# Optimization experiments

Hardware: AMD Instinct MI355X
Metric: run time of the kernel (lower is better)

Reference implementation:

```python
import jax, jax.numpy as jnp
import numpy as np

B, N, C, H, P = 16, 4096, 256, 4, 64  # batch, tokens, hidden, heads, proj_size
HD = C // H  # head dim = 64
EPS = 1e-12  # torch F.normalize eps


def _l2norm(t):
    # normalize along last axis, torch-style: t / max(||t||, eps)
    n = jnp.sqrt(jnp.sum(t * t, axis=-1, keepdims=True))
    return t / jnp.maximum(n, EPS)


def setup_inputs() -> dict:
    key = jax.random.key(0)
    ks = jax.random.split(key, 12)
    s = 0.02
    return {
        "x": jax.random.normal(ks[0], (B, N, C), jnp.float32),
        "ref": jax.random.normal(ks[1], (B, N, C), jnp.float32),
        "Wq": jax.random.normal(ks[2], (C, C), jnp.float32) * s,
        "bq": jnp.zeros((C,), jnp.float32),
        "Wkvv": jax.random.normal(ks[3], (3 * C, C), jnp.float32) * s,
        "bkvv": jnp.zeros((3 * C,), jnp.float32),
        "WE": jax.random.normal(ks[4], (P, N), jnp.float32) * s,  # E and F share weights
        "bE": jnp.zeros((P,), jnp.float32),
        "Wo1": jax.random.normal(ks[5], (C // 2, C), jnp.float32) * s,
        "bo1": jnp.zeros((C // 2,), jnp.float32),
        "Wo2": jax.random.normal(ks[6], (C // 2, C), jnp.float32) * s,
        "bo2": jnp.zeros((C // 2,), jnp.float32),
        "temp": jnp.ones((H, 1, 1), jnp.float32),
        "temp2": jnp.ones((H, 1, 1), jnp.float32),
    }


def reference(x, ref, Wq, bq, Wkvv, bkvv, WE, bE, Wo1, bo1, Wo2, bo2, temp, temp2):
    b, n, c = x.shape
    hd = c // H
    # q projection -> [B,H,hd,N] (already transposed so channel dim first)
    q = (x @ Wq.T + bq).reshape(b, n, H, hd).transpose(0, 2, 3, 1)
    kvv = (ref @ Wkvv.T + bkvv).reshape(b, n, 3, H, hd).transpose(2, 0, 3, 4, 1)
    k, v_ca, v_sa = kvv[0], kvv[1], kvv[2]
    # L2 normalize over token axis (last)
    qn = _l2norm(q)
    kn = _l2norm(k)
    # ---- channel attention (XCA-style): [B,H,hd,hd]
    attn_ca = jax.nn.softmax(jnp.einsum('bhcn,bhdn->bhcd', qn, kn) * temp, axis=-1)
    x_ca = jnp.einsum('bhcd,bhdn->bhcn', attn_ca, v_ca)  # [B,H,hd,N]
    x_ca = x_ca.transpose(0, 3, 1, 2).reshape(b, n, c)   # [B,N,C]
    # ---- spatial attention with Linformer-style projection (E == F shared)
    k_proj = kn @ WE.T + bE      # [B,H,hd,P]
    v_proj = v_sa @ WE.T + bE    # [B,H,hd,P]
    attn_sa = jax.nn.softmax(jnp.einsum('bhcn,bhcp->bhnp', qn, k_proj) * temp2, axis=-1)
    x_sa = jnp.einsum('bhnp,bhcp->bhnc', attn_sa, v_proj)  # [B,H,N,hd]
    # faithful to original permute(0,3,1,2).reshape(B,N,C)
    x_sa = x_sa.transpose(0, 3, 1, 2).reshape(b, n, c)
    # output projections + concat (SA first, then CA)
    out_ca = x_ca @ Wo1.T + bo1
    out_sa = x_sa @ Wo2.T + bo2
    return jnp.concatenate((out_sa, out_ca), axis=-1)
```

## Files before the change

### kernel.cpp

```cpp
#include <hip/hip_runtime.h>
#include <hip/hip_bf16.h>

#define DI __device__ __forceinline__

constexpr int B_ = 16, N_ = 4096, C_ = 256, H_ = 4;
constexpr size_t QSZ = (size_t)4096 * 4096;
constexpr int LDW = 72;
constexpr int LDC = 136;

typedef __attribute__((ext_vector_type(8))) short bh8;
typedef __attribute__((ext_vector_type(4))) float fx4;
typedef __attribute__((address_space(1))) unsigned int gu32;
typedef __attribute__((address_space(3))) unsigned int lu32;

DI float bfu2f(unsigned short u) { return __uint_as_float(((unsigned)u) << 16); }
DI void bfu2x2(unsigned u, float& lo, float& hi) {
  lo = __uint_as_float(u << 16);
  hi = __uint_as_float(u & 0xffff0000u);
}
DI unsigned short f2bfu(float f) {
  unsigned u = __float_as_uint(f);
  unsigned r = 0x7fffu + ((u >> 16) & 1u);
  return (unsigned short)((u + r) >> 16);
}
DI void gl_lds16(const unsigned short* g, unsigned short* l) {
  __builtin_amdgcn_global_load_lds((gu32*)g, (lu32*)l, 16, 0, 0);
}
DI int co_off(int row, int col) {
  const int o = col >> 3;
  const int so = (o & 8) | ((o & 7) ^ ((row >> 3) & 7));
  return row * LDC + so * 8 + (col & 7);
}

__global__ __launch_bounds__(256) void cast_xref(
    const float* __restrict__ x, const float* __restrict__ ref,
    unsigned short* __restrict__ xb, unsigned short* __restrict__ refb)
{
  const int bid = blockIdx.x;
  const float* src = (bid < 8192) ? x : ref;
  unsigned short* dst = (bid < 8192) ? xb : refb;
  const size_t base = ((size_t)(bid & 8191) * 256 + threadIdx.x) * 8;
  const float4 a = *reinterpret_cast<const float4*>(&src[base]);
  const float4 b = *reinterpret_cast<const float4*>(&src[base + 4]);
  union { uint4 v; unsigned short u[8]; } pk;
  pk.u[0] = f2bfu(a.x); pk.u[1] = f2bfu(a.y); pk.u[2] = f2bfu(a.z); pk.u[3] = f2bfu(a.w);
  pk.u[4] = f2bfu(b.x); pk.u[5] = f2bfu(b.y); pk.u[6] = f2bfu(b.z); pk.u[7] = f2bfu(b.w);
  *reinterpret_cast<uint4*>(&dst[base]) = pk.v;
}

__global__ __launch_bounds__(256) void cast_w(
    const float* __restrict__ Wq, const float* __restrict__ Wkvv,
    const float* __restrict__ Wo2, const float* __restrict__ Wo1,
    const float* __restrict__ WE, unsigned short* __restrict__ Wb,
    unsigned short* __restrict__ wEb)
{
  const int b = blockIdx.x;
  const float* src; unsigned short* dst; int lb;
  if (b < 32)       { src = Wq;   dst = Wb;          lb = b; }
  else if (b < 128) { src = Wkvv; dst = Wb + 65536;  lb = b - 32; }
  else if (b < 144) { src = Wo2;  dst = Wb + 262144; lb = b - 128; }
  else if (b < 160) { src = Wo1;  dst = Wb + 294912; lb = b - 144; }
  else              { src = WE;   dst = wEb;         lb = b - 160; }
  const size_t base = ((size_t)lb * 256 + threadIdx.x) * 8;
  const float4 a = *reinterpret_cast<const float4*>(&src[base]);
  const float4 bb = *reinterpret_cast<const float4*>(&src[base + 4]);
  union { uint4 v; unsigned short u[8]; } pk;
  pk.u[0] = f2bfu(a.x);  pk.u[1] = f2bfu(a.y);  pk.u[2] = f2bfu(a.z);  pk.u[3] = f2bfu(a.w);
  pk.u[4] = f2bfu(bb.x); pk.u[5] = f2bfu(bb.y); pk.u[6] = f2bfu(bb.z); pk.u[7] = f2bfu(bb.w);
  *reinterpret_cast<uint4*>(&dst[base]) = pk.v;
}

__global__ __launch_bounds__(256) void proj_fused(
    const unsigned short* __restrict__ xb, const unsigned short* __restrict__ refb,
    const unsigned short* __restrict__ Wball,
    const float* __restrict__ bq, const float* __restrict__ bkvv,
    unsigned short* __restrict__ qT, unsigned short* __restrict__ kvv2T,
    unsigned short* __restrict__ qtok, unsigned short* __restrict__ vtok)
{
  __shared__ unsigned short smem[17408];
  __shared__ float biasS[128];
  const int tid = threadIdx.x;
  const int lane = tid & 63, wid = tid >> 6;
  const int l15 = lane & 15, l4 = lane >> 4;
  const int wr = wid >> 1, wc = wid & 1;
  const int yt = blockIdx.y;
  const bool isq = (yt < 2);
  const unsigned short* Ab = isq ? xb : refb;
  const unsigned short* Wsrc = isq ? Wball : (Wball + 65536);
  const float* bias = isq ? bq : bkvv;
  unsigned short* outT = isq ? qT : kvv2T;
  const int j0 = (isq ? yt : (yt - 2)) * 128;
  const int pl = j0 >> 8;
  const bool writeT = isq || (pl != 1);
  const int plT = (!isq && pl == 2) ? 1 : 0;
  unsigned short* tok = isq ? qtok : ((pl == 1) ? vtok : nullptr);
  const int n0 = blockIdx.x * 128;
  const int b = blockIdx.z;
  const size_t tok0 = (size_t)b * 4096 + n0;
  const int lrow = lane >> 3, lcb = lane & 7;
  if (tid < 128) biasS[tid] = bias[j0 + tid];

  fx4 acc[4][4];
#pragma unroll
  for (int m = 0; m < 4; ++m)
#pragma unroll
    for (int n = 0; n < 4; ++n) acc[m][n] = (fx4){0.f, 0.f, 0.f, 0.f};

  auto STAGE = [&](int k0) {
    unsigned short* Wd = smem;
    unsigned short* Xd = smem + 8192;
#pragma unroll
    for (int i = 0; i < 4; ++i) {
      const int ci = i * 4 + wid;
      const int row = ci * 8 + lrow;
      const int scb = lcb ^ (row & 7);
      gl_lds16(&Wsrc[(size_t)(j0 + row) * 256 + k0 + scb * 8], &Wd[ci * 512]);
      gl_lds16(&Ab[(tok0 + row) * 256 + k0 + scb * 8], &Xd[ci * 512]);
    }
  };
  auto COMPUTE = [&]() {
    const unsigned short* Ws = smem;
    const unsigned short* Xs = smem + 8192;
#pragma unroll
    for (int kk = 0; kk < 2; ++kk) {
      const int cbi = kk * 4 + l4;
      bh8 af[4], bfr[4];
#pragma unroll
      for (int m = 0; m < 4; ++m) {
        const int r = wr * 64 + m * 16 + l15;
        af[m] = *reinterpret_cast<const bh8*>(&Ws[r * 64 + ((cbi ^ (r & 7)) << 3)]);
      }
#pragma unroll
      for (int n = 0; n < 4; ++n) {
        const int r = wc * 64 + n * 16 + l15;
        bfr[n] = *reinterpret_cast<const bh8*>(&Xs[r * 64 + ((cbi ^ (r & 7)) << 3)]);
      }
#pragma unroll
      for (int m = 0; m < 4; ++m)
#pragma unroll
        for (int n = 0; n < 4; ++n)
          acc[m][n] = __builtin_amdgcn_mfma_f32_16x16x32_bf16(af[m], bfr[n], acc[m][n], 0, 0, 0);
    }
  };

  for (int t = 0; t < 4; ++t) {
    STAGE(t * 64);
    __syncthreads();
    COMPUTE();
    __syncthreads();
  }

  unsigned short* Co = smem;
#pragma unroll
  for (int m = 0; m < 4; ++m) {
    const int jl = wr * 64 + m * 16 + (l4 << 2);
#pragma unroll
    for (int n = 0; n < 4; ++n) {
      const int col = wc * 64 + n * 16 + l15;
#pragma unroll
      for (int r = 0; r < 4; ++r) {
        const int row = jl + r;
        Co[co_off(row, col)] = f2bfu(acc[m][n][r] + biasS[row]);
      }
    }
  }
  __syncthreads();
  if (writeT) {
#pragma unroll
    for (int c = 0; c < 8; ++c) {
      const int r = c * 16 + (tid >> 4);
      const int colseg = (tid & 15) * 8;
      const uint4 v = *reinterpret_cast<const uint4*>(&Co[co_off(r, colseg)]);
      const int jj = j0 + r;
      const int rowT = (plT * B_ + b) * 256 + (jj & 255);
      *reinterpret_cast<uint4*>(&outT[(size_t)rowT * N_ + n0 + colseg]) = v;
    }
  }
  if (tok) {
    const int j = tid & 7;
#pragma unroll
    for (int i = 0; i < 8; ++i) {
      const int half = i >> 2;
      const int cb = half * 64 + j * 8;
      const int nloc = (i & 3) * 32 + (tid >> 3);
      union { uint4 v; unsigned short u[8]; } pk;
#pragma unroll
      for (int t = 0; t < 8; ++t)
        pk.u[t] = Co[co_off(cb + t, nloc)];
      const int jj = j0 + cb;
      const int hh = (jj >> 6) & 3, cc = jj & 63;
      *reinterpret_cast<uint4*>(
          &tok[(((size_t)b * 4 + hh) * 4096 + n0 + nloc) * 64 + cc]) = pk.v;
    }
  }
}

__global__ __launch_bounds__(256) void gemm_outm2(
    const unsigned short* __restrict__ Asa, const unsigned short* __restrict__ Aca,
    const unsigned short* __restrict__ Wob,
    const float* __restrict__ bo2, const float* __restrict__ bo1,
    float* __restrict__ out)
{
  __shared__ unsigned short smem[16384];
  __shared__ float biasS[128];
  const unsigned short* A = (blockIdx.z == 0) ? Asa : Aca;
  const unsigned short* Wsrc = Wob + (size_t)blockIdx.z * 32768;
  const float* bias = (blockIdx.z == 0) ? bo2 : bo1;
  const int joff = blockIdx.z * 128;
  const int tid = threadIdx.x;
  const int lane = tid & 63, wid = tid >> 6;
  const int l15 = lane & 15, l4 = lane >> 4;
  const int wr = wid >> 1, wc = wid & 1;
  const size_t m0 = (size_t)blockIdx.x * 128;
  const int lrow = lane >> 3, lcb = lane & 7;
  if (tid < 128) biasS[tid] = bias[tid];

  fx4 acc[4][4];
#pragma unroll
  for (int m = 0; m < 4; ++m)
#pragma unroll
    for (int n = 0; n < 4; ++n) acc[m][n] = (fx4){0.f, 0.f, 0.f, 0.f};

  auto STAGE = [&](int k0) {
    unsigned short* Wd = smem;
    unsigned short* Xd = smem + 8192;
#pragma unroll
    for (int i = 0; i < 4; ++i) {
      const int ci = i * 4 + wid;
      const int row = ci * 8 + lrow;
      const int scb = lcb ^ (row & 7);
      gl_lds16(&Wsrc[(size_t)row * 256 + k0 + scb * 8], &Wd[ci * 512]);
      gl_lds16(&A[(m0 + row) * 256 + k0 + scb * 8], &Xd[ci * 512]);
    }
  };
  auto COMPUTE = [&]() {
    const unsigned short* Ws = smem;
    const unsigned short* Xs = smem + 8192;
#pragma unroll
    for (int kk = 0; kk < 2; ++kk) {
      const int cbi = kk * 4 + l4;
      bh8 af[4], bfr[4];
#pragma unroll
      for (int m = 0; m < 4; ++m) {
        const int r = wr * 64 + m * 16 + l15;
        af[m] = *reinterpret_cast<const bh8*>(&Xs[r * 64 + ((cbi ^ (r & 7)) << 3)]);
      }
#pragma unroll
      for (int n = 0; n < 4; ++n) {
        const int r = wc * 64 + n * 16 + l15;
        bfr[n] = *reinterpret_cast<const bh8*>(&Ws[r * 64 + ((cbi ^ (r & 7)) << 3)]);
      }
#pragma unroll
      for (int m = 0; m < 4; ++m)
#pragma unroll
        for (int n = 0; n < 4; ++n)
          acc[m][n] = __builtin_amdgcn_mfma_f32_16x16x32_bf16(af[m], bfr[n], acc[m][n], 0, 0, 0);
    }
  };

  for (int t = 0; t < 4; ++t) {
    STAGE(t * 64);
    __syncthreads();
    COMPUTE();
    __syncthreads();
  }

#pragma unroll
  for (int mi = 0; mi < 4; ++mi) {
    const int mrow = wr * 64 + mi * 16 + (l4 << 2);
#pragma unroll
    for (int ni = 0; ni < 4; ++ni) {
      const int j = wc * 64 + ni * 16 + l15;
      const float bv = biasS[j];
#pragma unroll
      for (int r = 0; r < 4; ++r)
        out[(m0 + mrow + r) * 256 + joff + j] = acc[mi][ni][r] + bv;
    }
  }
}

__global__ __launch_bounds__(256) void stats_mfma(
    const unsigned short* __restrict__ qT, const unsigned short* __restrict__ kT,
    const unsigned short* __restrict__ vT, const unsigned short* __restrict__ wEb,
    float* __restrict__ part, float* __restrict__ partN)
{
  __shared__ unsigned short smem[4 * 64 * LDW];
  unsigned short* sq = smem;
  unsigned short* sk = smem + 64 * LDW;
  unsigned short* sv = smem + 2 * 64 * LDW;
  unsigned short* sw = smem + 3 * 64 * LDW;
  const int tid = threadIdx.x;
  const int lane = tid & 63, wid = tid >> 6;
  const int bh = blockIdx.x, chunk = blockIdx.y;
  const size_t rowbase = (size_t)bh * 64 * N_;

  fx4 acc[4][4];
#pragma unroll
  for (int m = 0; m < 4; ++m)
#pragma unroll
    for (int n = 0; n < 4; ++n) acc[m][n] = (fx4){0.f, 0.f, 0.f, 0.f};
  float q2 = 0.f, k2 = 0.f;

  const unsigned short* Aop = (wid == 1) ? sw : (wid == 2) ? sv : sq;
  const unsigned short* Bop = (wid == 1) ? sk : (wid == 2) ? sw : sk;

  for (int tile = 0; tile < 8; ++tile) {
    const int n0 = chunk * 512 + tile * 64;
#pragma unroll
    for (int c = 0; c < 2; ++c) {
      const int idx = c * 256 + tid;
      const int r = idx >> 3;
      const int off = (idx & 7) * 8;
      *reinterpret_cast<uint4*>(&sq[r * LDW + off]) =
          *reinterpret_cast<const uint4*>(&qT[rowbase + (size_t)r * N_ + n0 + off]);
      *reinterpret_cast<uint4*>(&sk[r * LDW + off]) =
          *reinterpret_cast<const uint4*>(&kT[rowbase + (size_t)r * N_ + n0 + off]);
      *reinterpret_cast<uint4*>(&sv[r * LDW + off]) =
          *reinterpret_cast<const uint4*>(&vT[rowbase + (size_t)r * N_ + n0 + off]);
      *reinterpret_cast<uint4*>(&sw[r * LDW + off]) =
          *reinterpret_cast<const uint4*>(&wEb[(size_t)r * N_ + n0 + off]);
    }
    __syncthreads();
    if (wid < 3) {
#pragma unroll
      for (int kk = 0; kk < 2; ++kk) {
        const int kb = kk * 32 + (lane >> 4) * 8;
        bh8 af[4], bfr[4];
#pragma unroll
        for (int m = 0; m < 4; ++m)
          af[m] = *reinterpret_cast<const bh8*>(&Aop[(m * 16 + (lane & 15)) * LDW + kb]);
#pragma unroll
        for (int n = 0; n < 4; ++n)
          bfr[n] = *reinterpret_cast<const bh8*>(&Bop[(n * 16 + (lane & 15)) * LDW + kb]);
#pragma unroll
        for (int m = 0; m < 4; ++m)
#pragma unroll
          for (int n = 0; n < 4; ++n)
            acc[m][n] = __builtin_amdgcn_mfma_f32_16x16x32_bf16(af[m], bfr[n], acc[m][n], 0, 0, 0);
      }
    } else {
      const unsigned short* qrow = &sq[lane * LDW];
      const unsigned short* krow = &sk[lane * LDW];
#pragma unroll
      for (int t = 0; t < 8; ++t) {
        const uint4 uq = *reinterpret_cast<const uint4*>(&qrow[t * 8]);
        const uint4 uk = *reinterpret_cast<const uint4*>(&krow[t * 8]);
        float a, b;
        bfu2x2(uq.x, a, b); q2 += a * a + b * b;
        bfu2x2(uq.y, a, b); q2 += a * a + b * b;
        bfu2x2(uq.z, a, b); q2 += a * a + b * b;
        bfu2x2(uq.w, a, b); q2 += a * a + b * b;
        bfu2x2(uk.x, a, b); k2 += a * a + b * b;
        bfu2x2(uk.y, a, b); k2 += a * a + b * b;
        bfu2x2(uk.z, a, b); k2 += a * a + b * b;
        bfu2x2(uk.w, a, b); k2 += a * a + b * b;
      }
    }
    __syncthreads();
  }

  if (wid < 3) {
    float* base = &part[(((size_t)chunk * 64 + bh) * 3 + wid) * 4096];
#pragma unroll
    for (int m = 0; m < 4; ++m) {
      const int row0 = m * 16 + ((lane >> 4) << 2);
#pragma unroll
      for (int n = 0; n < 4; ++n) {
        const int col = n * 16 + (lane & 15);
#pragma unroll
        for (int r = 0; r < 4; ++r)
          base[(row0 + r) * 64 + col] = acc[m][n][r];
      }
    }
  } else {
    float* nb = &partN[((size_t)chunk * 64 + bh) * 128];
    nb[lane] = q2;
    nb[64 + lane] = k2;
  }
}

__global__ __launch_bounds__(256) void postproc_kernel(
    const float* __restrict__ part, const float* __restrict__ partN,
    const float* __restrict__ bE,
    const float* __restrict__ temp, const float* __restrict__ temp2,
    unsigned short* __restrict__ attn_b,
    unsigned short* __restrict__ kp2t, unsigned short* __restrict__ vpb)
{
  __shared__ float sums[12288];
  __shared__ float rqS[64], rkS[64];
  const int bh = blockIdx.x;
  const int tid = threadIdx.x;
  for (int idx = tid; idx < 12288; idx += 256) {
    float s = 0.f;
    for (int ch = 0; ch < 8; ++ch)
      s += part[((size_t)ch * 64 + bh) * 12288 + idx];
    sums[idx] = s;
  }
  if (tid < 128) {
    float s = 0.f;
    for (int ch = 0; ch < 8; ++ch)
      s += partN[((size_t)ch * 64 + bh) * 128 + tid];
    const float r = 1.f / fmaxf(sqrtf(s), 1e-12f);
    if (tid < 64) rqS[tid] = r; else rkS[tid - 64] = r;
  }
  __syncthreads();
  const float t2 = temp2[bh & 3];
  for (int idx = tid; idx < 4096; idx += 256) {
    const int p = idx >> 6, c = idx & 63;
    kp2t[(size_t)bh * 4096 + idx] =
        f2bfu((sums[4096 + idx] * rkS[c] + bE[p]) * rqS[c] * t2);
    vpb[(size_t)bh * 4096 + idx] = f2bfu(sums[8192 + idx] + bE[idx & 63]);
  }
  const float tv = temp[bh & 3];
  const int lane = tid & 63, wv = tid >> 6;
  for (int ri = 0; ri < 16; ++ri) {
    const int c = wv * 16 + ri;
    const float val = sums[c * 64 + lane] * rqS[c] * rkS[lane] * tv;
    float m = val;
#pragma unroll
    for (int off = 32; off > 0; off >>= 1) m = fmaxf(m, __shfl_xor(m, off));
    const float e = __expf(val - m);
    float ssum = e;
#pragma unroll
    for (int off = 32; off > 0; off >>= 1) ssum += __shfl_xor(ssum, off);
    attn_b[(size_t)bh * 4096 + c * 64 + lane] = f2bfu(e / ssum);
  }
}

__global__ __launch_bounds__(256) void sa_mfma(
    const unsigned short* __restrict__ qtok, const unsigned short* __restrict__ kp2t,
    const unsigned short* __restrict__ vpb, unsigned short* __restrict__ x_sa)
{
  __shared__ unsigned short skp[64 * LDW];
  __shared__ unsigned short svp[64 * LDW];
  __shared__ unsigned short pt[4][64 * LDW];
  const int tid = threadIdx.x;
  const int lane = tid & 63, wid = tid >> 6;
  const int l15 = lane & 15, l4 = lane >> 4;
  const int bh = blockIdx.x, b = bh >> 2, h = bh & 3;
  const int n0 = blockIdx.y * 256 + wid * 64;
  unsigned short* myp = &pt[wid][0];

#pragma unroll
  for (int i = 0; i < 2; ++i) {
    const int idx = i * 256 + tid;
    const int r = idx >> 3, off = (idx & 7) * 8;
    *reinterpret_cast<uint4*>(&skp[r * LDW + off]) =
        *reinterpret_cast<const uint4*>(&kp2t[(size_t)bh * 4096 + r * 64 + off]);
    *reinterpret_cast<uint4*>(&svp[r * LDW + off]) =
        *reinterpret_cast<const uint4*>(&vpb[(size_t)bh * 4096 + r * 64 + off]);
  }
  __syncthreads();

  fx4 acc[4][4];
#pragma unroll
  for (int m = 0; m < 4; ++m)
#pragma unroll
    for (int j = 0; j < 4; ++j) acc[m][j] = (fx4){0.f, 0.f, 0.f, 0.f};
  const size_t qbase = ((size_t)bh * 4096 + n0) * 64;
#pragma unroll
  for (int kk = 0; kk < 2; ++kk) {
    const int kb = kk * 32 + l4 * 8;
    bh8 af[4], bf[4];
#pragma unroll
    for (int m = 0; m < 4; ++m)
      af[m] = *reinterpret_cast<const bh8*>(&qtok[qbase + (size_t)(m * 16 + l15) * 64 + kb]);
#pragma unroll
    for (int j = 0; j < 4; ++j)
      bf[j] = *reinterpret_cast<const bh8*>(&skp[(j * 16 + l15) * LDW + kb]);
#pragma unroll
    for (int m = 0; m < 4; ++m)
#pragma unroll
      for (int j = 0; j < 4; ++j)
        acc[m][j] = __builtin_amdgcn_mfma_f32_16x16x32_bf16(af[m], bf[j], acc[m][j], 0, 0, 0);
  }

  fx4 inv[4];
#pragma unroll
  for (int m = 0; m < 4; ++m) {
    fx4 vm = acc[m][0];
#pragma unroll
    for (int j = 1; j < 4; ++j)
#pragma unroll
      for (int r = 0; r < 4; ++r) vm[r] = fmaxf(vm[r], acc[m][j][r]);
#pragma unroll
    for (int msk = 1; msk < 16; msk <<= 1)
#pragma unroll
      for (int r = 0; r < 4; ++r) vm[r] = fmaxf(vm[r], __shfl_xor(vm[r], msk));
    fx4 s = (fx4){0.f, 0.f, 0.f, 0.f};
#pragma unroll
    for (int j = 0; j < 4; ++j)
#pragma unroll
      for (int r = 0; r < 4; ++r) {
        acc[m][j][r] = __expf(acc[m][j][r] - vm[r]);
        s[r] += acc[m][j][r];
      }
#pragma unroll
    for (int msk = 1; msk < 16; msk <<= 1)
#pragma unroll
      for (int r = 0; r < 4; ++r) s[r] += __shfl_xor(s[r], msk);
#pragma unroll
    for (int r = 0; r < 4; ++r) inv[m][r] = 1.f / s[r];
#pragma unroll
    for (int j = 0; j < 4; ++j)
#pragma unroll
      for (int r = 0; r < 4; ++r)
        myp[(m * 16 + l4 * 4 + r) * LDW + j * 16 + l15] = f2bfu(acc[m][j][r]);
  }

  fx4 acc2[4][4];
#pragma unroll
  for (int m = 0; m < 4; ++m)
#pragma unroll
    for (int j = 0; j < 4; ++j) acc2[m][j] = (fx4){0.f, 0.f, 0.f, 0.f};
#pragma unroll
  for (int kk = 0; kk < 2; ++kk) {
    const int kb = kk * 32 + l4 * 8;
    bh8 af[4], bf[4];
#pragma unroll
    for (int m = 0; m < 4; ++m)
      af[m] = *reinterpret_cast<const bh8*>(&myp[(m * 16 + l15) * LDW + kb]);
#pragma unroll
    for (int j = 0; j < 4; ++j)
      bf[j] = *reinterpret_cast<const bh8*>(&svp[(j * 16 + l15) * LDW + kb]);
#pragma unroll
    for (int m = 0; m < 4; ++m)
#pragma unroll
      for (int j = 0; j < 4; ++j)
        acc2[m][j] = __builtin_amdgcn_mfma_f32_16x16x32_bf16(af[m], bf[j], acc2[m][j], 0, 0, 0);
  }

#pragma unroll
  for (int m = 0; m < 4; ++m)
#pragma unroll
    for (int j = 0; j < 4; ++j)
#pragma unroll
      for (int r = 0; r < 4; ++r)
        myp[(m * 16 + l4 * 4 + r) * 65 + j * 16 + l15] = f2bfu(acc2[m][j][r] * inv[m][r]);
#pragma unroll
  for (int dstep = 0; dstep < 8; ++dstep) {
    const int d = dstep * 8 + (lane >> 3);
    const int nseg = (lane & 7) * 8;
    union { uint4 v; unsigned short u[8]; } pk;
#pragma unroll
    for (int t = 0; t < 8; ++t) pk.u[t] = myp[(nseg + t) * 65 + d];
    *reinterpret_cast<uint4*>(
        &x_sa[((size_t)(b * 64 + d) * 4 + h) * (size_t)N_ + n0 + nseg]) = pk.v;
  }
}

__global__ __launch_bounds__(256) void xca_mfma(
    const unsigned short* __restrict__ attn_b, const unsigned short* __restrict__ vtok,
    unsigned short* __restrict__ x_ca)
{
  __shared__ unsigned short co[4][64 * LDW];
  const int tid = threadIdx.x;
  const int lane = tid & 63, wid = tid >> 6;
  const int l15 = lane & 15, l4 = lane >> 4;
  const int bh = blockIdx.x, b = bh >> 2, h = bh & 3;
  const int n0 = blockIdx.y * 256 + wid * 64;
  unsigned short* myco = &co[wid][0];

  fx4 acc[4][4];
#pragma unroll
  for (int m = 0; m < 4; ++m)
#pragma unroll
    for (int j = 0; j < 4; ++j) acc[m][j] = (fx4){0.f, 0.f, 0.f, 0.f};
  const size_t abase = (size_t)bh * 4096;
  const size_t vbase = ((size_t)bh * 4096 + n0) * 64;
#pragma unroll
  for (int kk = 0; kk < 2; ++kk) {
    const int kb = kk * 32 + l4 * 8;
    bh8 af[4], bf[4];
#pragma unroll
    for (int m = 0; m < 4; ++m)
      af[m] = *reinterpret_cast<const bh8*>(&attn_b[abase + (size_t)(m * 16 + l15) * 64 + kb]);
#pragma unroll
    for (int j = 0; j < 4; ++j)
      bf[j] = *reinterpret_cast<const bh8*>(&vtok[vbase + (size_t)(j * 16 + l15) * 64 + kb]);
#pragma unroll
    for (int m = 0; m < 4; ++m)
#pragma unroll
      for (int j = 0; j < 4; ++j)
        acc[m][j] = __builtin_amdgcn_mfma_f32_16x16x32_bf16(af[m], bf[j], acc[m][j], 0, 0, 0);
  }

#pragma unroll
  for (int m = 0; m < 4; ++m)
#pragma unroll
    for (int j = 0; j < 4; ++j)
#pragma unroll
      for (int r = 0; r < 4; ++r)
        myco[(j * 16 + l15) * LDW + m * 16 + l4 * 4 + r] = f2bfu(acc[m][j][r]);
#pragma unroll
  for (int p = 0; p < 8; ++p) {
    const int nloc = p * 8 + (lane >> 3);
    const int cseg = (lane & 7) * 8;
    const uint4 v = *reinterpret_cast<const uint4*>(&myco[nloc * LDW + cseg]);
    *reinterpret_cast<uint4*>(
        &x_ca[((size_t)b * N_ + n0 + nloc) * 256 + h * 64 + cseg]) = v;
  }
}

extern "C" void kernel_launch(void* const* d_in, const int* in_sizes, int n_in,
                              void* d_out, int out_size, void* d_ws, size_t ws_size,
                              hipStream_t stream)
{
  const float* x     = (const float*)d_in[0];
  const float* ref   = (const float*)d_in[1];
  const float* Wq    = (const float*)d_in[2];
  const float* bq    = (const float*)d_in[3];
  const float* Wkvv  = (const float*)d_in[4];
  const float* bkvv  = (const float*)d_in[5];
  const float* WE    = (const float*)d_in[6];
  const float* bE    = (const float*)d_in[7];
  const float* Wo1   = (const float*)d_in[8];
  const float* bo1   = (const float*)d_in[9];
  const float* Wo2   = (const float*)d_in[10];
  const float* bo2   = (const float*)d_in[11];
  const float* temp  = (const float*)d_in[12];
  const float* temp2 = (const float*)d_in[13];
  float* out = (float*)d_out;

  char* ws = (char*)d_ws;
  unsigned short* qT      = (unsigned short*)(ws);
  unsigned short* kvv2T   = (unsigned short*)(ws + 33554432);
  unsigned short* qtok    = (unsigned short*)(ws + 100663296);
  unsigned short* refb    = (unsigned short*)(ws + 134217728);
  unsigned short* x_sa    = (unsigned short*)(ws + 134217728);
  unsigned short* vca_tok = (unsigned short*)(ws + 167772160);
  unsigned short* xb      = (unsigned short*)(ws + 201326592);
  float*          part    = (float*)(ws + 201326592);
  unsigned short* x_ca    = (unsigned short*)(ws + 201326592);
  float*          partN   = (float*)(ws + 226492416);
  unsigned short* Wb      = (unsigned short*)(ws + 234881024);
  unsigned short* wEb     = (unsigned short*)(ws + 235536384);
  unsigned short* attn_b  = (unsigned short*)(ws + 236093440);
  unsigned short* kp2t    = (unsigned short*)(ws + 236617728);
  unsigned short* vpb     = (unsigned short*)(ws + 237142016);

  const dim3 blk(256);
  cast_xref<<<dim3(16384), blk, 0, stream>>>(x, ref, xb, refb);
  cast_w<<<dim3(288), blk, 0, stream>>>(Wq, Wkvv, Wo2, Wo1, WE, Wb, wEb);
  proj_fused<<<dim3(32, 8, 16), blk, 0, stream>>>(xb, refb, Wb, bq, bkvv,
                                                  qT, kvv2T, qtok, vca_tok);
  stats_mfma<<<dim3(64, 8), blk, 0, stream>>>(qT, kvv2T, kvv2T + QSZ, wEb, part, partN);
  postproc_kernel<<<dim3(64), blk, 0, stream>>>(part, partN, bE, temp, temp2,
                                                attn_b, kp2t, vpb);
  sa_mfma<<<dim3(64, 16), blk, 0, stream>>>(qtok, kp2t, vpb, x_sa);
  xca_mfma<<<dim3(64, 16), blk, 0, stream>>>(attn_b, vca_tok, x_ca);
  gemm_outm2<<<dim3(512, 1, 2), blk, 0, stream>>>(x_sa, x_ca, Wb + 262144, bo2, bo1, out);
}
```

Measured before the change: 205.2 us.

## Merge cast kernels and remap projection grid for XCD-aware L2 reuse

The two fp32-to-bf16 cast kernels become one launch covering activations and weights, which removes one kernel launch. The projection GEMM switches from a 3D grid to a 1D grid. Its block index is decoded so that the eight output-column tiles for the same token tile land on the same XCD, which should let them share that XCD's L2 for the input tile. The index remap is arithmetic only, but a wrong decode would silently produce a partial result.

```diff
diff --git a/kernel.cpp b/kernel.cpp
--- a/kernel.cpp
+++ b/kernel.cpp
@@ -32,35 +32,26 @@
   return row * LDC + so * 8 + (col & 7);
 }
 
-__global__ __launch_bounds__(256) void cast_xref(
+__global__ __launch_bounds__(256) void cast_all(
     const float* __restrict__ x, const float* __restrict__ ref,
-    unsigned short* __restrict__ xb, unsigned short* __restrict__ refb)
-{
-  const int bid = blockIdx.x;
-  const float* src = (bid < 8192) ? x : ref;
-  unsigned short* dst = (bid < 8192) ? xb : refb;
-  const size_t base = ((size_t)(bid & 8191) * 256 + threadIdx.x) * 8;
-  const float4 a = *reinterpret_cast<const float4*>(&src[base]);
-  const float4 b = *reinterpret_cast<const float4*>(&src[base + 4]);
-  union { uint4 v; unsigned short u[8]; } pk;
-  pk.u[0] = f2bfu(a.x); pk.u[1] = f2bfu(a.y); pk.u[2] = f2bfu(a.z); pk.u[3] = f2bfu(a.w);
-  pk.u[4] = f2bfu(b.x); pk.u[5] = f2bfu(b.y); pk.u[6] = f2bfu(b.z); pk.u[7] = f2bfu(b.w);
-  *reinterpret_cast<uint4*>(&dst[base]) = pk.v;
-}
-
-__global__ __launch_bounds__(256) void cast_w(
     const float* __restrict__ Wq, const float* __restrict__ Wkvv,
     const float* __restrict__ Wo2, const float* __restrict__ Wo1,
-    const float* __restrict__ WE, unsigned short* __restrict__ Wb,
-    unsigned short* __restrict__ wEb)
-{
-  const int b = blockIdx.x;
+    const float* __restrict__ WE,
+    unsigned short* __restrict__ xb, unsigned short* __restrict__ refb,
+    unsigned short* __restrict__ Wb, unsigned short* __restrict__ wEb)
+{
+  const int bid = blockIdx.x;
   const float* src; unsigned short* dst; int lb;
-  if (b < 32)       { src = Wq;   dst = Wb;          lb = b; }
-  else if (b < 128) { src = Wkvv; dst = Wb + 65536;  lb = b - 32; }
-  else if (b < 144) { src = Wo2;  dst = Wb + 262144; lb = b - 128; }
-  else if (b < 160) { src = Wo1;  dst = Wb + 294912; lb = b - 144; }
-  else              { src = WE;   dst = wEb;         lb = b - 160; }
+  if (bid < 8192)       { src = x;    dst = xb;          lb = bid; }
+  else if (bid < 16384) { src = ref;  dst = refb;        lb = bid - 8192; }
+  else {
+    const int b = bid - 16384;
+    if (b < 32)       { src = Wq;   dst = Wb;          lb = b; }
+    else if (b < 128) { src = Wkvv; dst = Wb + 65536;  lb = b - 32; }
+    else if (b < 144) { src = Wo2;  dst = Wb + 262144; lb = b - 128; }
+    else if (b < 160) { src = Wo1;  dst = Wb + 294912; lb = b - 144; }
+    else              { src = WE;   dst = wEb;         lb = b - 160; }
+  }
   const size_t base = ((size_t)lb * 256 + threadIdx.x) * 8;
   const float4 a = *reinterpret_cast<const float4*>(&src[base]);
   const float4 bb = *reinterpret_cast<const float4*>(&src[base + 4]);
@@ -83,7 +74,13 @@
   const int lane = tid & 63, wid = tid >> 6;
   const int l15 = lane & 15, l4 = lane >> 4;
   const int wr = wid >> 1, wc = wid & 1;
-  const int yt = blockIdx.y;
+  const int lin = blockIdx.x;
+  const int xcd = lin & 7;
+  const int s = lin >> 3;
+  const int yt = s & 7;
+  const int G = (s >> 3) * 8 + xcd;
+  const int xi = G & 31;
+  const int b = G >> 5;
   const bool isq = (yt < 2);
   const unsigned short* Ab = isq ? xb : refb;
   const unsigned short* Wsrc = isq ? Wball : (Wball + 65536);
@@ -94,8 +91,7 @@
   const bool writeT = isq || (pl != 1);
   const int plT = (!isq && pl == 2) ? 1 : 0;
   unsigned short* tok = isq ? qtok : ((pl == 1) ? vtok : nullptr);
-  const int n0 = blockIdx.x * 128;
-  const int b = blockIdx.z;
+  const int n0 = xi * 128;
   const size_t tok0 = (size_t)b * 4096 + n0;
   const int lrow = lane >> 3, lcb = lane & 7;
   if (tid < 128) biasS[tid] = bias[j0 + tid];
@@ -640,10 +636,10 @@
   unsigned short* vpb     = (unsigned short*)(ws + 237142016);
 
   const dim3 blk(256);
-  cast_xref<<<dim3(16384), blk, 0, stream>>>(x, ref, xb, refb);
-  cast_w<<<dim3(288), blk, 0, stream>>>(Wq, Wkvv, Wo2, Wo1, WE, Wb, wEb);
-  proj_fused<<<dim3(32, 8, 16), blk, 0, stream>>>(xb, refb, Wb, bq, bkvv,
-                                                  qT, kvv2T, qtok, vca_tok);
+  cast_all<<<dim3(16672), blk, 0, stream>>>(x, ref, Wq, Wkvv, Wo2, Wo1, WE,
+                                            xb, refb, Wb, wEb);
+  proj_fused<<<dim3(4096), blk, 0, stream>>>(xb, refb, Wb, bq, bkvv,
+                                             qT, kvv2T, qtok, vca_tok);
   stats_mfma<<<dim3(64, 8), blk, 0, stream>>>(qT, kvv2T, kvv2T + QSZ, wEb, part, partN);
   postproc_kernel<<<dim3(64), blk, 0, stream>>>(part, partN, bE, temp, temp2,
                                                 attn_b, kp2t, vpb);
```

Result: no change. 202.7 us (median of 2 runs) (-1.2%).
